# Optimization experiments

Measured on AMD Instinct MI355X. Metric: run time of the kernel, lower is better.

## Reference

```python
import jax, jax.numpy as jnp
import numpy as np

N, E = 50000, 600000
IN_DIM, HID, OUT_DIM = 128, 256, 64


def _sage_conv(x, edge_index, W_l, W_r, b):
    # PyG SAGEConv (mean aggr, root_weight=True):
    # out = mean_{j in N(i)} x_j @ W_l + x_i @ W_r + b
    src, dst = edge_index[0], edge_index[1]
    msg = x[src]  # [E, d] gather
    agg = jax.ops.segment_sum(msg, dst, num_segments=N)  # [N, d]
    cnt = jax.ops.segment_sum(jnp.ones((E,), dtype=x.dtype), dst, num_segments=N)
    agg = agg / jnp.maximum(cnt, 1.0)[:, None]
    return agg @ W_l + x @ W_r + b


def setup_inputs() -> dict:
    key = jax.random.key(0)
    ks = jax.random.split(key, 8)
    x = jax.random.normal(ks[0], (N, IN_DIM), dtype=jnp.float32)
    edge_index = jax.random.randint(ks[1], (2, E), 0, N, dtype=jnp.int64)
    s1 = 1.0 / np.sqrt(IN_DIM)
    s2 = 1.0 / np.sqrt(HID)
    W1_l = jax.random.uniform(ks[2], (IN_DIM, HID), jnp.float32, -s1, s1)
    W1_r = jax.random.uniform(ks[3], (IN_DIM, HID), jnp.float32, -s1, s1)
    b1 = jnp.zeros((HID,), jnp.float32)
    W2_l = jax.random.uniform(ks[4], (HID, OUT_DIM), jnp.float32, -s2, s2)
    W2_r = jax.random.uniform(ks[5], (HID, OUT_DIM), jnp.float32, -s2, s2)
    b2 = jnp.zeros((OUT_DIM,), jnp.float32)
    return {"x": x, "edge_index": edge_index, "W1_l": W1_l, "W1_r": W1_r,
            "b1": b1, "W2_l": W2_l, "W2_r": W2_r, "b2": b2}


def reference(x, edge_index, W1_l, W1_r, b1, W2_l, W2_r, b2):
    # SAGE.forward, eval mode (dropout = identity)
    h = jax.nn.relu(_sage_conv(x, edge_index, W1_l, W1_r, b1))
    out = _sage_conv(h, edge_index, W2_l, W2_r, b2)
    return out
```

## Files before the change

kernel.cpp:

```cpp
#include <hip/hip_runtime.h>

#define N_NODES 50000
#define N_EDGES 600000
#define N_PAD   50048
#define IN_DIM 128
#define HID 256
#define OUT_DIM 64
#define MAX_DEG 64

typedef __attribute__((ext_vector_type(4))) float f32x4;
typedef __attribute__((ext_vector_type(8))) short short8;
typedef unsigned short u16;
typedef unsigned int u32;

__device__ __forceinline__ float bf2f(u32 lo16) {
  u32 u = lo16 << 16;
  return __builtin_bit_cast(float, u);
}
__device__ __forceinline__ u16 f2bf(float f) {
  u32 u = __builtin_bit_cast(u32, f);
  u = (u + 0x7FFF + ((u >> 16) & 1)) >> 16;
  return (u16)u;
}

#define SEG0 (N_PAD * 16)
#define SEG1 (SEG0 + 256 * 256)
#define SEG2 (SEG1 + 128 * 256)
#define SEG3 (SEG2 + N_NODES)
#define PREP_TOT SEG3

__global__ void k_prep(const float* __restrict__ x,
                       const float* __restrict__ W1l, const float* __restrict__ W1r,
                       const float* __restrict__ W2l, const float* __restrict__ W2r,
                       u16* __restrict__ xb, u16* __restrict__ W1t,
                       u16* __restrict__ W2t, int* __restrict__ cnt) {
  int idx = blockIdx.x * 256 + threadIdx.x;
  if (idx < SEG0) {
    int row = idx >> 4;
    int c8 = (idx & 15) * 8;
    short8 o;
    if (row < N_NODES) {
      f32x4 a = *(const f32x4*)&x[(size_t)row * 128 + c8];
      f32x4 b = *(const f32x4*)&x[(size_t)row * 128 + c8 + 4];
      o[0] = (short)f2bf(a[0]); o[1] = (short)f2bf(a[1]);
      o[2] = (short)f2bf(a[2]); o[3] = (short)f2bf(a[3]);
      o[4] = (short)f2bf(b[0]); o[5] = (short)f2bf(b[1]);
      o[6] = (short)f2bf(b[2]); o[7] = (short)f2bf(b[3]);
    } else {
      for (int j = 0; j < 8; ++j) o[j] = 0;
    }
    *(short8*)&xb[(size_t)row * 128 + c8] = o;
  } else if (idx < SEG1) {
    int i = idx - SEG0;
    int nn = i >> 8, k = i & 255;
    float v = (k < 128) ? W1l[(size_t)k * HID + nn] : W1r[(size_t)(k - 128) * HID + nn];
    W1t[(size_t)nn * 256 + k] = f2bf(v);
  } else if (idx < SEG2) {
    int i = idx - SEG1;
    int nn = i >> 8, k = i & 255;
    float v = (nn < 64) ? W2l[(size_t)k * OUT_DIM + nn]
                        : W2r[(size_t)k * OUT_DIM + (nn - 64)];
    W2t[(size_t)nn * 256 + k] = f2bf(v);
  } else if (idx < SEG3) {
    cnt[idx - SEG2] = 0;
  }
}


__global__ void k_fill(const int* __restrict__ src, const int* __restrict__ dst,
                       int* __restrict__ cnt, int* __restrict__ bucket) {
  int e = blockIdx.x * 256 + threadIdx.x;
  if (e < N_EDGES) {
    int d = dst[e];
    int pos = atomicAdd(&cnt[d], 1);
    if (pos < MAX_DEG) bucket[(size_t)d * MAX_DEG + pos] = src[e];
  }
}


__global__ void k_agg(const u16* __restrict__ xb, const int* __restrict__ cnt,
                      const int* __restrict__ bucket, u16* __restrict__ agg) {
  int node = blockIdx.x * 4 + (threadIdx.x >> 6);
  if (node >= N_PAD) return;
  int lane = threadIdx.x & 63;
  int es = lane >> 4, dl = lane & 15;
  int deg = (node < N_NODES) ? cnt[node] : 0;
  int sreg = (node < N_NODES) ? bucket[(size_t)node * MAX_DEG + lane] : 0;
  float acc[8] = {0.f, 0.f, 0.f, 0.f, 0.f, 0.f, 0.f, 0.f};
  for (int e = 0; e < deg; e += 4) {
    int ee = e + es;
    int s = __shfl(sreg, ee & 63);
    if (ee < deg) {
      short8 v = *(const short8*)&xb[(size_t)s * 128 + dl * 8];
#pragma unroll
      for (int j = 0; j < 8; ++j) acc[j] += bf2f((u16)v[j]);
    }
  }
#pragma unroll
  for (int j = 0; j < 8; ++j) {
    acc[j] += __shfl_xor(acc[j], 16);
    acc[j] += __shfl_xor(acc[j], 32);
  }
  float inv = 1.f / fmaxf((float)deg, 1.f);
  if (es == 0) {
    short8 o;
#pragma unroll
    for (int j = 0; j < 8; ++j) o[j] = (short)f2bf(acc[j] * inv);
    *(short8*)&agg[(size_t)node * 128 + dl * 8] = o;
  }
}


__device__ __forceinline__ void gl_lds16(const void* g, void* l) {
  __builtin_amdgcn_global_load_lds((const __attribute__((address_space(1))) u32*)g,
                                   (__attribute__((address_space(3))) u32*)l, 16, 0, 0);
}

__global__ __launch_bounds__(256, 2) void k_mlp(
    const u16* __restrict__ agg, const u16* __restrict__ xb,
    const u16* __restrict__ W1t, const u16* __restrict__ W2t,
    const float* __restrict__ b1, u16* __restrict__ pb, u16* __restrict__ qb) {
  __shared__ u16 hs[64 * 256];
  __shared__ u16 As[2][64 * 64];
  __shared__ u16 Bs[256 * 64];
  const int t = threadIdx.x;
  const int wave = t >> 6;
  const int lane = t & 63;
  const int brow = blockIdx.x * 64;
  const int lr = lane & 15;
  const int kg = lane >> 4;

  const int wr = (wave >> 1) * 32;
  const int wc = (wave & 1) * 128;

  f32x4 acc[2][8];
#pragma unroll
  for (int m = 0; m < 2; ++m)
#pragma unroll
    for (int n = 0; n < 8; ++n) acc[m][n] = (f32x4){0.f, 0.f, 0.f, 0.f};

  auto stageA = [&](int buf, int kt) {
    const u16* base = (kt < 2) ? agg : xb;
    const int koff = (kt & 1) * 64;
#pragma unroll
    for (int i = 0; i < 2; ++i) {
      int chunk = wave * 2 + i;
      int f = chunk * 1024 + lane * 16;
      int row = f >> 7;
      int cbs = (f & 127) ^ ((row & 7) << 4);
      gl_lds16(&base[(size_t)(brow + row) * 128 + koff + (cbs >> 1)],
               (char*)As[buf] + chunk * 1024);
    }
  };
  auto stageB = [&](int kt) {
    const int k0 = kt * 64;
#pragma unroll
    for (int i = 0; i < 8; ++i) {
      int chunk = wave * 8 + i;
      int f = chunk * 1024 + lane * 16;
      int row = f >> 7;
      int cbs = (f & 127) ^ ((row & 7) << 4);
      gl_lds16(&W1t[(size_t)row * 256 + k0 + (cbs >> 1)],
               (char*)Bs + chunk * 1024);
    }
  };

  stageA(0, 0);
  stageB(0);
  __syncthreads();

#pragma unroll
  for (int kt = 0; kt < 4; ++kt) {
    const int cur = kt & 1;
    if (kt < 3) stageA(cur ^ 1, kt + 1);
#pragma unroll
    for (int kk = 0; kk < 2; ++kk) {
      short8 af[2], bfr[8];
      const int cb = kk * 64 + kg * 16;
#pragma unroll
      for (int m = 0; m < 2; ++m) {
        int row = wr + m * 16 + lr;
        af[m] = *(const short8*)((const char*)As[cur] + row * 128 + (cb ^ ((row & 7) << 4)));
      }
#pragma unroll
      for (int n = 0; n < 8; ++n) {
        int row = wc + n * 16 + lr;
        bfr[n] = *(const short8*)((const char*)Bs + row * 128 + (cb ^ ((row & 7) << 4)));
      }
#pragma unroll
      for (int m = 0; m < 2; ++m)
#pragma unroll
        for (int n = 0; n < 8; ++n)
          acc[m][n] =
              __builtin_amdgcn_mfma_f32_16x16x32_bf16(af[m], bfr[n], acc[m][n], 0, 0, 0);
    }
    __syncthreads();
    if (kt < 3) {
      stageB(kt + 1);
      __syncthreads();
    }
  }

#pragma unroll
  for (int n = 0; n < 8; ++n) {
    int col = wc + n * 16 + lr;
    float bv = b1[col];
#pragma unroll
    for (int m = 0; m < 2; ++m) {
#pragma unroll
      for (int j = 0; j < 4; ++j) {
        int row = wr + kg * 4 + m * 16 + j;
        float v = fmaxf(acc[m][n][j] + bv, 0.f);
        *(u16*)((char*)hs + row * 512 + ((col * 2) ^ ((row & 7) << 4))) = f2bf(v);
      }
    }
  }
  __syncthreads();

  const int wr2 = (wave >> 1) * 32;
  const int wc2 = (wave & 1) * 64;
  f32x4 acc2[2][4];
#pragma unroll
  for (int m = 0; m < 2; ++m)
#pragma unroll
    for (int n = 0; n < 4; ++n) acc2[m][n] = (f32x4){0.f, 0.f, 0.f, 0.f};

#pragma unroll
  for (int kk = 0; kk < 8; ++kk) {
    const int cb = kk * 64 + kg * 16;
    short8 af[2], bfr[4];
#pragma unroll
    for (int m = 0; m < 2; ++m) {
      int row = wr2 + m * 16 + lr;
      af[m] = *(const short8*)((const char*)hs + row * 512 + (cb ^ ((row & 7) << 4)));
    }
#pragma unroll
    for (int n = 0; n < 4; ++n) {
      int row = wc2 + n * 16 + lr;
      bfr[n] = *(const short8*)&W2t[(size_t)row * 256 + kk * 32 + kg * 8];
    }
#pragma unroll
    for (int m = 0; m < 2; ++m)
#pragma unroll
      for (int n = 0; n < 4; ++n)
        acc2[m][n] =
            __builtin_amdgcn_mfma_f32_16x16x32_bf16(af[m], bfr[n], acc2[m][n], 0, 0, 0);
  }

  u16* outb = (wave & 1) ? qb : pb;
#pragma unroll
  for (int n = 0; n < 4; ++n) {
    int col = (wc2 + n * 16 + lr) & 63;
#pragma unroll
    for (int m = 0; m < 2; ++m) {
#pragma unroll
      for (int j = 0; j < 4; ++j) {
        int row = brow + wr2 + kg * 4 + m * 16 + j;
        outb[(size_t)row * 64 + col] = f2bf(acc2[m][n][j]);
      }
    }
  }
}


__global__ void k_out(const u16* __restrict__ pb, const u16* __restrict__ qb,
                      const int* __restrict__ cnt, const int* __restrict__ bucket,
                      const float* __restrict__ b2, float* __restrict__ out) {
  int node = blockIdx.x * 4 + (threadIdx.x >> 6);
  if (node >= N_NODES) return;
  int lane = threadIdx.x & 63;
  int es = lane >> 3, dl = lane & 7;
  int deg = cnt[node];
  int sreg = bucket[(size_t)node * MAX_DEG + lane];
  float acc[8] = {0.f, 0.f, 0.f, 0.f, 0.f, 0.f, 0.f, 0.f};
  for (int e = 0; e < deg; e += 8) {
    int ee = e + es;
    int s = __shfl(sreg, ee & 63);
    if (ee < deg) {
      short8 v = *(const short8*)&pb[(size_t)s * 64 + dl * 8];
#pragma unroll
      for (int j = 0; j < 8; ++j) acc[j] += bf2f((u16)v[j]);
    }
  }
#pragma unroll
  for (int j = 0; j < 8; ++j) {
    acc[j] += __shfl_xor(acc[j], 8);
    acc[j] += __shfl_xor(acc[j], 16);
    acc[j] += __shfl_xor(acc[j], 32);
  }
  float inv = 1.f / fmaxf((float)deg, 1.f);
  if (es == 0) {
    short8 q = *(const short8*)&qb[(size_t)node * 64 + dl * 8];
    f32x4 bb0 = *(const f32x4*)&b2[dl * 8];
    f32x4 bb1 = *(const f32x4*)&b2[dl * 8 + 4];
    f32x4 o0, o1;
#pragma unroll
    for (int j = 0; j < 4; ++j) {
      o0[j] = acc[j] * inv + bf2f((u16)q[j]) + bb0[j];
      o1[j] = acc[j + 4] * inv + bf2f((u16)q[j + 4]) + bb1[j];
    }
    *(f32x4*)&out[(size_t)node * 64 + dl * 8] = o0;
    *(f32x4*)&out[(size_t)node * 64 + dl * 8 + 4] = o1;
  }
}


extern "C" void kernel_launch(void* const* d_in, const int* in_sizes, int n_in,
                              void* d_out, int out_size, void* d_ws, size_t ws_size,
                              hipStream_t stream) {
  const float* x   = (const float*)d_in[0];
  const int*   ei  = (const int*)d_in[1];
  const float* W1l = (const float*)d_in[2];
  const float* W1r = (const float*)d_in[3];
  const float* b1  = (const float*)d_in[4];
  const float* W2l = (const float*)d_in[5];
  const float* W2r = (const float*)d_in[6];
  const float* b2  = (const float*)d_in[7];
  float* out = (float*)d_out;

  const int* src = ei;
  const int* dst = ei + N_EDGES;

  char* ws = (char*)d_ws;
  size_t off = 0;
  auto alloc = [&](size_t bytes) -> void* {
    void* p = ws + off;
    off = (off + bytes + 255) & ~(size_t)255;
    return p;
  };
  int* cnt    = (int*)alloc((size_t)N_NODES * 4);
  int* bucket = (int*)alloc((size_t)N_NODES * MAX_DEG * 4);
  u16* xb     = (u16*)alloc((size_t)N_PAD * 128 * 2);
  u16* agg    = (u16*)alloc((size_t)N_PAD * 128 * 2);
  u16* W1t    = (u16*)alloc((size_t)256 * 256 * 2);
  u16* W2t    = (u16*)alloc((size_t)128 * 256 * 2);
  u16* pb     = (u16*)alloc((size_t)N_PAD * 64 * 2);
  u16* qb     = (u16*)alloc((size_t)N_PAD * 64 * 2);

  k_prep<<<(PREP_TOT + 255) / 256, 256, 0, stream>>>(x, W1l, W1r, W2l, W2r,
                                                     xb, W1t, W2t, cnt);
  k_fill<<<(N_EDGES + 255) / 256, 256, 0, stream>>>(src, dst, cnt, bucket);
  k_agg<<<N_PAD / 4, 256, 0, stream>>>(xb, cnt, bucket, agg);
  k_mlp<<<N_PAD / 64, 256, 0, stream>>>(agg, xb, W1t, W2t, b1, pb, qb);
  k_out<<<(N_NODES + 3) / 4, 256, 0, stream>>>(pb, qb, cnt, bucket, b2, out);
}
```

Before: 121.1 us.

## Pre-pack weights in MFMA fragment order and drop LDS staging of B

```diff
diff --git a/kernel.cpp b/kernel.cpp
--- a/kernel.cpp
+++ b/kernel.cpp
@@ -24,16 +24,16 @@
 }
 
 #define SEG0 (N_PAD * 16)
-#define SEG1 (SEG0 + 256 * 256)
-#define SEG2 (SEG1 + 128 * 256)
+#define SEG1 (SEG0 + 128 * 64)
+#define SEG2 (SEG1 + 64 * 64)
 #define SEG3 (SEG2 + N_NODES)
 #define PREP_TOT SEG3
 
 __global__ void k_prep(const float* __restrict__ x,
                        const float* __restrict__ W1l, const float* __restrict__ W1r,
                        const float* __restrict__ W2l, const float* __restrict__ W2r,
-                       u16* __restrict__ xb, u16* __restrict__ W1t,
-                       u16* __restrict__ W2t, int* __restrict__ cnt) {
+                       u16* __restrict__ xb, u16* __restrict__ W1p,
+                       u16* __restrict__ W2p, int* __restrict__ cnt) {
   int idx = blockIdx.x * 256 + threadIdx.x;
   if (idx < SEG0) {
     int row = idx >> 4;
@@ -52,15 +52,33 @@
     *(short8*)&xb[(size_t)row * 128 + c8] = o;
   } else if (idx < SEG1) {
     int i = idx - SEG0;
-    int nn = i >> 8, k = i & 255;
-    float v = (k < 128) ? W1l[(size_t)k * HID + nn] : W1r[(size_t)(k - 128) * HID + nn];
-    W1t[(size_t)nn * 256 + k] = f2bf(v);
+    int F = i >> 6, l = i & 63;
+    int wch = F >> 6, kt = (F >> 4) & 3, kk = (F >> 3) & 1, n = F & 7;
+    int row = wch * 128 + n * 16 + (l & 15);
+    int kb = kt * 64 + kk * 32 + (l >> 4) * 8;
+    short8 o;
+#pragma unroll
+    for (int j = 0; j < 8; ++j) {
+      int k = kb + j;
+      float v = (k < 128) ? W1l[(size_t)k * HID + row] : W1r[(size_t)(k - 128) * HID + row];
+      o[j] = (short)f2bf(v);
+    }
+    *(short8*)&W1p[(size_t)i * 8] = o;
   } else if (idx < SEG2) {
     int i = idx - SEG1;
-    int nn = i >> 8, k = i & 255;
-    float v = (nn < 64) ? W2l[(size_t)k * OUT_DIM + nn]
-                        : W2r[(size_t)k * OUT_DIM + (nn - 64)];
-    W2t[(size_t)nn * 256 + k] = f2bf(v);
+    int G = i >> 6, l = i & 63;
+    int wch = G >> 5, kk = (G >> 2) & 7, n = G & 3;
+    int row = wch * 64 + n * 16 + (l & 15);
+    int kb = kk * 32 + (l >> 4) * 8;
+    short8 o;
+#pragma unroll
+    for (int j = 0; j < 8; ++j) {
+      int k = kb + j;
+      float v = (row < 64) ? W2l[(size_t)k * OUT_DIM + row]
+                           : W2r[(size_t)k * OUT_DIM + (row - 64)];
+      o[j] = (short)f2bf(v);
+    }
+    *(short8*)&W2p[(size_t)i * 8] = o;
   } else if (idx < SEG3) {
     cnt[idx - SEG2] = 0;
   }
@@ -87,15 +105,18 @@
   int deg = (node < N_NODES) ? cnt[node] : 0;
   int sreg = (node < N_NODES) ? bucket[(size_t)node * MAX_DEG + lane] : 0;
   float acc[8] = {0.f, 0.f, 0.f, 0.f, 0.f, 0.f, 0.f, 0.f};
+  short8 pend = (short8){0, 0, 0, 0, 0, 0, 0, 0};
   for (int e = 0; e < deg; e += 4) {
     int ee = e + es;
     int s = __shfl(sreg, ee & 63);
-    if (ee < deg) {
-      short8 v = *(const short8*)&xb[(size_t)s * 128 + dl * 8];
-#pragma unroll
-      for (int j = 0; j < 8; ++j) acc[j] += bf2f((u16)v[j]);
-    }
-  }
+    short8 v = (short8){0, 0, 0, 0, 0, 0, 0, 0};
+    if (ee < deg) v = *(const short8*)&xb[(size_t)s * 128 + dl * 8];
+#pragma unroll
+    for (int j = 0; j < 8; ++j) acc[j] += bf2f((u16)pend[j]);
+    pend = v;
+  }
+#pragma unroll
+  for (int j = 0; j < 8; ++j) acc[j] += bf2f((u16)pend[j]);
 #pragma unroll
   for (int j = 0; j < 8; ++j) {
     acc[j] += __shfl_xor(acc[j], 16);
@@ -116,22 +137,22 @@
                                    (__attribute__((address_space(3))) u32*)l, 16, 0, 0);
 }
 
-__global__ __launch_bounds__(256, 2) void k_mlp(
+__global__ __launch_bounds__(256, 3) void k_mlp(
     const u16* __restrict__ agg, const u16* __restrict__ xb,
-    const u16* __restrict__ W1t, const u16* __restrict__ W2t,
+    const u16* __restrict__ W1p, const u16* __restrict__ W2p,
     const float* __restrict__ b1, u16* __restrict__ pb, u16* __restrict__ qb) {
   __shared__ u16 hs[64 * 256];
   __shared__ u16 As[2][64 * 64];
-  __shared__ u16 Bs[256 * 64];
   const int t = threadIdx.x;
   const int wave = t >> 6;
   const int lane = t & 63;
   const int brow = blockIdx.x * 64;
   const int lr = lane & 15;
   const int kg = lane >> 4;
+  const int wch = wave & 1;
 
   const int wr = (wave >> 1) * 32;
-  const int wc = (wave & 1) * 128;
+  const int wc = wch * 128;
 
   f32x4 acc[2][8];
 #pragma unroll
@@ -152,21 +173,8 @@
                (char*)As[buf] + chunk * 1024);
     }
   };
-  auto stageB = [&](int kt) {
-    const int k0 = kt * 64;
-#pragma unroll
-    for (int i = 0; i < 8; ++i) {
-      int chunk = wave * 8 + i;
-      int f = chunk * 1024 + lane * 16;
-      int row = f >> 7;
-      int cbs = (f & 127) ^ ((row & 7) << 4);
-      gl_lds16(&W1t[(size_t)row * 256 + k0 + (cbs >> 1)],
-               (char*)Bs + chunk * 1024);
-    }
-  };
 
   stageA(0, 0);
-  stageB(0);
   __syncthreads();
 
 #pragma unroll
@@ -183,10 +191,9 @@
         af[m] = *(const short8*)((const char*)As[cur] + row * 128 + (cb ^ ((row & 7) << 4)));
       }
 #pragma unroll
-      for (int n = 0; n < 8; ++n) {
-        int row = wc + n * 16 + lr;
-        bfr[n] = *(const short8*)((const char*)Bs + row * 128 + (cb ^ ((row & 7) << 4)));
-      }
+      for (int n = 0; n < 8; ++n)
+        bfr[n] = *(const short8*)&W1p[(size_t)(((wch * 4 + kt) * 2 + kk) * 8 + n) * 512 +
+                                      lane * 8];
 #pragma unroll
       for (int m = 0; m < 2; ++m)
 #pragma unroll
@@ -195,10 +202,6 @@
               __builtin_amdgcn_mfma_f32_16x16x32_bf16(af[m], bfr[n], acc[m][n], 0, 0, 0);
     }
     __syncthreads();
-    if (kt < 3) {
-      stageB(kt + 1);
-      __syncthreads();
-    }
   }
 
 #pragma unroll
@@ -218,7 +221,6 @@
   __syncthreads();
 
   const int wr2 = (wave >> 1) * 32;
-  const int wc2 = (wave & 1) * 64;
   f32x4 acc2[2][4];
 #pragma unroll
   for (int m = 0; m < 2; ++m)
@@ -235,10 +237,8 @@
       af[m] = *(const short8*)((const char*)hs + row * 512 + (cb ^ ((row & 7) << 4)));
     }
 #pragma unroll
-    for (int n = 0; n < 4; ++n) {
-      int row = wc2 + n * 16 + lr;
-      bfr[n] = *(const short8*)&W2t[(size_t)row * 256 + kk * 32 + kg * 8];
-    }
+    for (int n = 0; n < 4; ++n)
+      bfr[n] = *(const short8*)&W2p[(size_t)((wch * 8 + kk) * 4 + n) * 512 + lane * 8];
 #pragma unroll
     for (int m = 0; m < 2; ++m)
 #pragma unroll
@@ -247,10 +247,10 @@
             __builtin_amdgcn_mfma_f32_16x16x32_bf16(af[m], bfr[n], acc2[m][n], 0, 0, 0);
   }
 
-  u16* outb = (wave & 1) ? qb : pb;
+  u16* outb = wch ? qb : pb;
 #pragma unroll
   for (int n = 0; n < 4; ++n) {
-    int col = (wc2 + n * 16 + lr) & 63;
+    int col = n * 16 + lr;
 #pragma unroll
     for (int m = 0; m < 2; ++m) {
 #pragma unroll
@@ -273,15 +273,18 @@
   int deg = cnt[node];
   int sreg = bucket[(size_t)node * MAX_DEG + lane];
   float acc[8] = {0.f, 0.f, 0.f, 0.f, 0.f, 0.f, 0.f, 0.f};
+  short8 pend = (short8){0, 0, 0, 0, 0, 0, 0, 0};
   for (int e = 0; e < deg; e += 8) {
     int ee = e + es;
     int s = __shfl(sreg, ee & 63);
-    if (ee < deg) {
-      short8 v = *(const short8*)&pb[(size_t)s * 64 + dl * 8];
-#pragma unroll
-      for (int j = 0; j < 8; ++j) acc[j] += bf2f((u16)v[j]);
-    }
-  }
+    short8 v = (short8){0, 0, 0, 0, 0, 0, 0, 0};
+    if (ee < deg) v = *(const short8*)&pb[(size_t)s * 64 + dl * 8];
+#pragma unroll
+    for (int j = 0; j < 8; ++j) acc[j] += bf2f((u16)pend[j]);
+    pend = v;
+  }
+#pragma unroll
+  for (int j = 0; j < 8; ++j) acc[j] += bf2f((u16)pend[j]);
 #pragma unroll
   for (int j = 0; j < 8; ++j) {
     acc[j] += __shfl_xor(acc[j], 8);
@@ -332,15 +335,15 @@
   int* bucket = (int*)alloc((size_t)N_NODES * MAX_DEG * 4);
   u16* xb     = (u16*)alloc((size_t)N_PAD * 128 * 2);
   u16* agg    = (u16*)alloc((size_t)N_PAD * 128 * 2);
-  u16* W1t    = (u16*)alloc((size_t)256 * 256 * 2);
-  u16* W2t    = (u16*)alloc((size_t)128 * 256 * 2);
+  u16* W1p    = (u16*)alloc((size_t)128 * 64 * 8 * 2);
+  u16* W2p    = (u16*)alloc((size_t)64 * 64 * 8 * 2);
   u16* pb     = (u16*)alloc((size_t)N_PAD * 64 * 2);
   u16* qb     = (u16*)alloc((size_t)N_PAD * 64 * 2);
 
   k_prep<<<(PREP_TOT + 255) / 256, 256, 0, stream>>>(x, W1l, W1r, W2l, W2r,
-                                                     xb, W1t, W2t, cnt);
+                                                     xb, W1p, W2p, cnt);
   k_fill<<<(N_EDGES + 255) / 256, 256, 0, stream>>>(src, dst, cnt, bucket);
   k_agg<<<N_PAD / 4, 256, 0, stream>>>(xb, cnt, bucket, agg);
-  k_mlp<<<N_PAD / 64, 256, 0, stream>>>(agg, xb, W1t, W2t, b1, pb, qb);
+  k_mlp<<<N_PAD / 64, 256, 0, stream>>>(agg, xb, W1p, W2p, b1, pb, qb);
   k_out<<<(N_NODES + 3) / 4, 256, 0, stream>>>(pb, qb, cnt, bucket, b2, out);
 }
```

Result: faster. 112.4 us (-7.2%).
